# Optimization experiments

Measured on AMD Instinct MI355X. Metric: run time of the kernel, lower is better.

## Reference

```python
import jax, jax.numpy as jnp
import numpy as np

N_NODES = 327680      # 8192 graphs * 40 nodes/graph
N_EDGES = 2621440     # avg degree 8
NODES_PER_GRAPH = 40


def _lin(k, fan_in, fan_out):
    s = 1.0 / np.sqrt(fan_in)
    return jax.random.uniform(k, (fan_in, fan_out), jnp.float32, -s, s)


def setup_inputs() -> dict:
    key = jax.random.key(0)
    ks = jax.random.split(key, 12)
    x = jax.random.normal(ks[0], (N_NODES, 58), jnp.float32)
    edge_index = jax.random.randint(ks[1], (2, N_EDGES), 0, N_NODES, dtype=jnp.int32)
    return {
        "x": x,
        "edge_index": edge_index,
        "W1": _lin(ks[2], 58, 96),  "b1": jnp.zeros((96,), jnp.float32),
        "W2": _lin(ks[3], 96, 48),  "b2": jnp.zeros((48,), jnp.float32),
        "l1_w": _lin(ks[4], 40 * 48, 256), "l1_b": jnp.zeros((256,), jnp.float32),
        "l2_w": _lin(ks[5], 256, 64),      "l2_b": jnp.zeros((64,), jnp.float32),
        "l3_w": _lin(ks[6], 64, 1),        "l3_b": jnp.zeros((1,), jnp.float32),
    }


def gcn_conv(x, src, dst, W, b, n):
    # PyG GCNConv: h = X W; out[i] = sum_{(j->i)} d_j^-1/2 d_i^-1/2 h[j] + b
    h = x @ W                                   # [N, out]
    deg = jnp.zeros((n,), h.dtype).at[dst].add(1.0)
    dinv = jnp.where(deg > 0, jax.lax.rsqrt(deg), 0.0)
    norm = dinv[src] * dinv[dst]                # [E]
    out = jax.ops.segment_sum(h[src] * norm[:, None], dst, num_segments=n)
    return out + b


def reference(x, edge_index, W1, b1, W2, b2, l1_w, l1_b, l2_w, l2_b, l3_w, l3_b):
    n = x.shape[0]
    loop = jnp.arange(n, dtype=edge_index.dtype)        # self-loops (PyG default)
    src = jnp.concatenate([edge_index[0], loop])
    dst = jnp.concatenate([edge_index[1], loop])
    h = jax.nn.relu(gcn_conv(x, src, dst, W1, b1, n))   # dropout is identity in eval
    h = jax.nn.relu(gcn_conv(h, src, dst, W2, b2, n))
    g = h.reshape(n // NODES_PER_GRAPH, NODES_PER_GRAPH * 48)
    g = jax.nn.relu(g @ l1_w + l1_b)
    g = jax.nn.relu(g @ l2_w + l2_b)
    return jax.nn.sigmoid(g @ l3_w + l3_b)              # [B, 1]
```

## Files before the change

kernel.cpp:

```cpp
#include <hip/hip_runtime.h>

#define N_NODES 327680
#define N_EDGES 2621440
#define NGRAPH  8192
#define NB      640
#define BCAPE   4608

typedef unsigned int uint;
typedef unsigned short u16;
typedef __attribute__((ext_vector_type(8))) short s16x8;
typedef __attribute__((ext_vector_type(4))) float f32x4;

__device__ __forceinline__ float bl(uint u){ return __uint_as_float(u << 16); }
__device__ __forceinline__ float bh(uint u){ return __uint_as_float(u & 0xffff0000u); }
__device__ __forceinline__ u16 f2b(float f){
    uint u = __float_as_uint(f);
    u += 0x7fffu + ((u>>16)&1u);
    return (u16)(u>>16);
}
__device__ __forceinline__ uint pk(float a, float b){
    return (uint)f2b(a) | ((uint)f2b(b) << 16);
}


__device__ void tr_tile(const float* __restrict__ in, u16* __restrict__ out,
                        int K, int N, int Kpad, int kb, int nb){
    __shared__ u16 t[64][72];
    for (int i = threadIdx.x; i < 4096; i += 256){
        int k = i >> 6, n = i & 63;
        int gk = kb + k, gn = nb + n;
        float v = (gk < K && gn < N) ? in[(size_t)gk*N + gn] : 0.f;
        t[n][k] = f2b(v);
    }
    __syncthreads();
    for (int i = threadIdx.x; i < 4096; i += 256){
        int n = i >> 6, k = i & 63;
        int gk = kb + k, gn = nb + n;
        if (gn < N && gk < Kpad) out[(size_t)gn*Kpad + gk] = t[n][k];
    }
}

__global__ __launch_bounds__(256) void k_prep(
    const float* __restrict__ W1, const float* __restrict__ W2,
    const float* __restrict__ l1w, const float* __restrict__ l2w,
    u16* __restrict__ w1t, u16* __restrict__ w2t,
    u16* __restrict__ l1wt, u16* __restrict__ l2wt, int* __restrict__ gcur)
{
    int b = blockIdx.x;
    if (b < 120)      tr_tile(l1w, l1wt, 1920, 256, 1920, (b%30)*64, (b/30)*64);
    else if (b < 124) tr_tile(l2w, l2wt, 256,  64,  256,  (b-120)*64, 0);
    else if (b < 126) tr_tile(W1,  w1t,  58,   96,  64,   0, (b-124)*64);
    else if (b < 128) tr_tile(W2,  w2t,  96,   48,  96,   (b-126)*64, 0);
    else {
        for (int i = threadIdx.x; i < NB; i += 256) gcur[i] = 0;
    }
}


__global__ __launch_bounds__(256) void k_partition(
    const int* __restrict__ src, const int* __restrict__ dst,
    int* __restrict__ gcur, uint* __restrict__ staging)
{
    __shared__ int cnt[NB], base_[NB];
    int tid = threadIdx.x;
    for (int i = tid; i < NB; i += 256) cnt[i] = 0;
    __syncthreads();
    int e0 = blockIdx.x*4096;
    int d[16];
    #pragma unroll
    for (int j = 0; j < 16; ++j){
        d[j] = dst[e0 + j*256 + tid];
        atomicAdd(&cnt[d[j] >> 9], 1);
    }
    __syncthreads();
    for (int i = tid; i < NB; i += 256)
        base_[i] = atomicAdd(&gcur[i], cnt[i]);
    __syncthreads();
    for (int i = tid; i < NB; i += 256) cnt[i] = 0;
    __syncthreads();
    #pragma unroll
    for (int j = 0; j < 16; ++j){
        int e = e0 + j*256 + tid;
        int b = d[j] >> 9;
        int r = atomicAdd(&cnt[b], 1);
        staging[(uint)b*BCAPE + base_[b] + r] = (uint)src[e] | ((uint)(d[j] & 511) << 19);
    }
}


__global__ __launch_bounds__(512) void k_bucket(
    const uint* __restrict__ staging, const int* __restrict__ gcur,
    int* __restrict__ rowst, int* __restrict__ rendg, float* __restrict__ dinvg,
    int* __restrict__ csr, int* __restrict__ perm)
{
    __shared__ uint sedge[BCAPE];
    __shared__ int deg[512];
    __shared__ int sc[512];
    __shared__ int cur[512];
    __shared__ int dh[64], dbase[64];
    const int b = blockIdx.x;
    const int tid = threadIdx.x;
    const int lo = b*BCAPE;
    int cnt = gcur[b];
    if (cnt > BCAPE) cnt = BCAPE;
    deg[tid] = 0;
    if (tid < 64) dh[tid] = 0;
    __syncthreads();
    for (int t = tid; t < cnt; t += 512){
        uint ed = staging[lo + t];
        sedge[t] = ed;
        atomicAdd(&deg[ed >> 19], 1);
    }
    __syncthreads();
    int d = deg[tid];
    sc[tid] = d;
    __syncthreads();
    for (int o = 1; o < 512; o <<= 1){
        int v = (tid >= o) ? sc[tid-o] : 0;
        __syncthreads();
        sc[tid] += v;
        __syncthreads();
    }
    int incl = sc[tid];
    int excl = incl - d;
    int gnode = b*512 + tid;
    rowst[gnode] = lo + excl;
    rendg[gnode] = lo + incl;
    dinvg[gnode] = 1.0f / sqrtf((float)(d + 1));
    cur[tid] = lo + excl;
    int bin = min(d, 63);
    atomicAdd(&dh[bin], 1);
    __syncthreads();
    if (tid == 0){
        int a = 0;
        #pragma unroll
        for (int i = 0; i < 64; ++i){ dbase[i] = a; a += dh[i]; dh[i] = 0; }
    }
    __syncthreads();
    int pos = dbase[bin] + atomicAdd(&dh[bin], 1);
    perm[b*512 + pos] = gnode;
    for (int t = tid; t < cnt; t += 512){
        uint ed = sedge[t];
        int p = atomicAdd(&cur[ed >> 19], 1);
        csr[p] = (int)(ed & 0x7FFFFu);
    }
}


__global__ void k_prescale2(const float* __restrict__ x, const float* __restrict__ dinv,
                            uint* __restrict__ xs32){
    int gid = blockIdx.x*256 + threadIdx.x;
    int node = gid >> 5, c = gid & 31;
    float dv = dinv[node];
    float a = 0.f, b = 0.f;
    if (c < 29){
        float2 v = *(const float2*)&x[(size_t)node*58 + 2*c];
        a = v.x * dv; b = v.y * dv;
    }
    xs32[(size_t)node*32 + c] = pk(a, b);
}


template<int BR>
__global__ __launch_bounds__(256) void k_gatherv(
    const int* __restrict__ rs, const int* __restrict__ re,
    const int* __restrict__ csr, const float* __restrict__ dinv,
    const int* __restrict__ perm,
    const uint4* __restrict__ feat4,
    const float* __restrict__ bias,
    u16* __restrict__ out)
{
    int slot = (blockIdx.x*256 + threadIdx.x) >> 3;
    int c4 = threadIdx.x & 7;
    int node = perm[slot];
    uint4 u = feat4[((uint)node << 3) + c4];
    float a0 = bl(u.x), a1 = bh(u.x), a2 = bl(u.y), a3 = bh(u.y);
    float a4 = bl(u.z), a5 = bh(u.z), a6 = bl(u.w), a7 = bh(u.w);
    int e = rs[node];
    const int e1 = re[node];
    while (e < e1){
        const int last = e1 - 1;
        int idx[8];
        #pragma unroll
        for (int k = 0; k < 8; ++k) idx[k] = csr[min(e + k, last)];
        uint4 uu[8];
        #pragma unroll
        for (int k = 0; k < 8; ++k) uu[k] = feat4[((uint)idx[k] << 3) + c4];
        #pragma unroll
        for (int k = 0; k < 8; ++k){
            if (e + k < e1){
                a0 += bl(uu[k].x); a1 += bh(uu[k].x);
                a2 += bl(uu[k].y); a3 += bh(uu[k].y);
                a4 += bl(uu[k].z); a5 += bh(uu[k].z);
                a6 += bl(uu[k].w); a7 += bh(uu[k].w);
            }
        }
        e += 8;
    }
    float di = dinv[node];
    a0 *= di; a1 *= di; a2 *= di; a3 *= di;
    a4 *= di; a5 *= di; a6 *= di; a7 *= di;
    if (BR){
        if (c4 < 6){
            float4 bz0 = *(const float4*)&bias[8*c4];
            float4 bz1 = *(const float4*)&bias[8*c4 + 4];
            a0 = fmaxf(a0 + bz0.x, 0.f); a1 = fmaxf(a1 + bz0.y, 0.f);
            a2 = fmaxf(a2 + bz0.z, 0.f); a3 = fmaxf(a3 + bz0.w, 0.f);
            a4 = fmaxf(a4 + bz1.x, 0.f); a5 = fmaxf(a5 + bz1.y, 0.f);
            a6 = fmaxf(a6 + bz1.z, 0.f); a7 = fmaxf(a7 + bz1.w, 0.f);
            uint4 w;
            w.x = pk(a0,a1); w.y = pk(a2,a3); w.z = pk(a4,a5); w.w = pk(a6,a7);
            *(uint4*)&out[(size_t)node*48 + c4*8] = w;
        }
    } else {
        uint4 w;
        w.x = pk(a0,a1); w.y = pk(a2,a3); w.z = pk(a4,a5); w.w = pk(a6,a7);
        *(uint4*)&out[(size_t)node*64 + c4*8] = w;
    }
}


__global__ __launch_bounds__(256) void k_conv_mlp(
    const u16* __restrict__ A,
    const u16* __restrict__ w1t,
    const float* __restrict__ b1,
    const u16* __restrict__ w2t,
    const float* __restrict__ dinv,
    u16* __restrict__ ts)
{
    __shared__ __align__(16) u16 As[64][72];
    __shared__ __align__(16) u16 Bt1[96][72];
    __shared__ __align__(16) u16 Bt2[48][104];
    __shared__ __align__(16) u16 sh1[64][104];
    __shared__ float sb1[96];
    const int tid = threadIdx.x;
    {
        const u16* Ab = A + (size_t)blockIdx.x*64*64;
        for (int i = tid; i < 512; i += 256){
            int r = i >> 3, s = i & 7;
            *(uint4*)&As[r][s*8] = *(const uint4*)&Ab[r*64 + s*8];
        }
    }
    for (int i = tid; i < 768; i += 256){
        int n = i >> 3, s = i & 7;
        *(uint4*)&Bt1[n][s*8] = *(const uint4*)&w1t[n*64 + s*8];
    }
    for (int i = tid; i < 576; i += 256){
        int n = i / 12, s = i % 12;
        *(uint4*)&Bt2[n][s*8] = *(const uint4*)&w2t[n*96 + s*8];
    }
    if (tid < 96) sb1[tid] = b1[tid];
    __syncthreads();

    const int wv = tid >> 6, l = tid & 63;
    const int lr = l & 15, lg = l >> 4;
    const int r0 = wv*16;

    f32x4 acc1[6] = {};
    #pragma unroll
    for (int s = 0; s < 2; ++s){
        s16x8 af = *(const s16x8*)&As[r0+lr][s*32 + lg*8];
        #pragma unroll
        for (int t = 0; t < 6; ++t){
            s16x8 bf = *(const s16x8*)&Bt1[t*16+lr][s*32 + lg*8];
            acc1[t] = __builtin_amdgcn_mfma_f32_16x16x32_bf16(af, bf, acc1[t], 0, 0, 0);
        }
    }
    #pragma unroll
    for (int t = 0; t < 6; ++t){
        int col = t*16 + lr;
        float bias = sb1[col];
        #pragma unroll
        for (int r = 0; r < 4; ++r)
            sh1[r0 + lg*4 + r][col] = f2b(fmaxf(acc1[t][r] + bias, 0.f));
    }
    __syncthreads();

    f32x4 acc2[3] = {};
    #pragma unroll
    for (int s = 0; s < 3; ++s){
        s16x8 af = *(const s16x8*)&sh1[r0+lr][s*32 + lg*8];
        #pragma unroll
        for (int t = 0; t < 3; ++t){
            s16x8 bf = *(const s16x8*)&Bt2[t*16+lr][s*32 + lg*8];
            acc2[t] = __builtin_amdgcn_mfma_f32_16x16x32_bf16(af, bf, acc2[t], 0, 0, 0);
        }
    }
    size_t gbase = (size_t)blockIdx.x*64;
    #pragma unroll
    for (int r = 0; r < 4; ++r){
        size_t row = gbase + r0 + lg*4 + r;
        float dv = dinv[row];
        #pragma unroll
        for (int t = 0; t < 3; ++t)
            ts[row*64 + t*16 + lr] = f2b(acc2[t][r] * dv);
        ts[row*64 + 48 + lr] = 0;
    }
}


__global__ __launch_bounds__(256) void k_head(
    const u16* __restrict__ A,
    const u16* __restrict__ l1wt,
    const float* __restrict__ l1b,
    const u16* __restrict__ l2wt,
    const float* __restrict__ l2b,
    const float* __restrict__ l3w, const float* __restrict__ l3b,
    float* __restrict__ out)
{
    __shared__ __align__(16) u16 As[32][72];
    __shared__ __align__(16) u16 Bt[256][72];
    __shared__ float part[32][2];
    u16 (*sh1)[264] = (u16(*)[264])&Bt[0][0];
    const int tid = threadIdx.x;
    const int g0 = blockIdx.x*32;
    const int w = tid >> 6, l = tid & 63;
    const int lr = l & 15, lg = l >> 4;
    const int r0 = (w & 1)*16;
    const int c0 = (w >> 1)*128;
    f32x4 acc[8] = {};
    for (int k0 = 0; k0 < 1920; k0 += 64){
        __syncthreads();
        {
            int r = tid >> 3, s = tid & 7;
            *(uint4*)&As[r][s*8] = *(const uint4*)&A[(size_t)(g0+r)*1920 + k0 + s*8];
        }
        for (int i = tid; i < 2048; i += 256){
            int n = i >> 3, s = i & 7;
            *(uint4*)&Bt[n][s*8] = *(const uint4*)&l1wt[(size_t)n*1920 + k0 + s*8];
        }
        __syncthreads();
        #pragma unroll
        for (int s = 0; s < 2; ++s){
            s16x8 af = *(const s16x8*)&As[r0+lr][s*32 + lg*8];
            #pragma unroll
            for (int t = 0; t < 8; ++t){
                s16x8 bf = *(const s16x8*)&Bt[c0 + t*16 + lr][s*32 + lg*8];
                acc[t] = __builtin_amdgcn_mfma_f32_16x16x32_bf16(af, bf, acc[t], 0, 0, 0);
            }
        }
    }
    __syncthreads();
    #pragma unroll
    for (int t = 0; t < 8; ++t){
        int col = c0 + t*16 + lr;
        float bs = l1b[col];
        #pragma unroll
        for (int r = 0; r < 4; ++r)
            sh1[r0 + lg*4 + r][col] = f2b(fmaxf(acc[t][r] + bs, 0.f));
    }
    __syncthreads();
    f32x4 acc2[2] = {};
    #pragma unroll
    for (int s = 0; s < 8; ++s){
        s16x8 af = *(const s16x8*)&sh1[r0+lr][s*32 + lg*8];
        #pragma unroll
        for (int t = 0; t < 2; ++t){
            int col = (w>>1)*32 + t*16 + lr;
            s16x8 bf = *(const s16x8*)&l2wt[(size_t)col*256 + s*32 + lg*8];
            acc2[t] = __builtin_amdgcn_mfma_f32_16x16x32_bf16(af, bf, acc2[t], 0, 0, 0);
        }
    }
    float p[4];
    #pragma unroll
    for (int r = 0; r < 4; ++r){
        p[r] = 0.f;
        #pragma unroll
        for (int t = 0; t < 2; ++t){
            int col = (w>>1)*32 + t*16 + lr;
            p[r] += fmaxf(acc2[t][r] + l2b[col], 0.f) * l3w[col];
        }
    }
    #pragma unroll
    for (int o = 1; o < 16; o <<= 1){
        #pragma unroll
        for (int r = 0; r < 4; ++r) p[r] += __shfl_xor(p[r], o);
    }
    if (lr == 0){
        #pragma unroll
        for (int r = 0; r < 4; ++r)
            part[r0 + lg*4 + r][w>>1] = p[r];
    }
    __syncthreads();
    if (tid < 32)
        out[g0 + tid] = 1.0f / (1.0f + expf(-(part[tid][0] + part[tid][1] + l3b[0])));
}

extern "C" void kernel_launch(void* const* d_in, const int* in_sizes, int n_in,
                              void* d_out, int out_size, void* d_ws, size_t ws_size,
                              hipStream_t stream){
    const float* x   = (const float*)d_in[0];
    const int*   ei  = (const int*)  d_in[1];
    const int*   src = ei;
    const int*   dst = ei + N_EDGES;
    const float* W1  = (const float*)d_in[2];
    const float* b1  = (const float*)d_in[3];
    const float* W2  = (const float*)d_in[4];
    const float* b2  = (const float*)d_in[5];
    const float* l1w = (const float*)d_in[6];
    const float* l1b = (const float*)d_in[7];
    const float* l2w = (const float*)d_in[8];
    const float* l2b = (const float*)d_in[9];
    const float* l3w = (const float*)d_in[10];
    const float* l3b = (const float*)d_in[11];
    float* out = (float*)d_out;

    char* w = (char*)d_ws;
    auto alloc = [&](size_t bytes){ void* p = (void*)w; w += (bytes + 255) & ~(size_t)255; return p; };
    float* dinv   = (float*)alloc((size_t)N_NODES*4);
    int*   rowst  = (int*)  alloc((size_t)N_NODES*4);
    int*   rend   = (int*)  alloc((size_t)N_NODES*4);
    int*   perm   = (int*)  alloc((size_t)N_NODES*4);
    int*   gcur   = (int*)  alloc(NB*4);
    u16*   w1t    = (u16*)  alloc(96*64*2);
    u16*   w2t    = (u16*)  alloc(48*96*2);
    u16*   l1wt   = (u16*)  alloc((size_t)256*1920*2);
    u16*   l2wt   = (u16*)  alloc((size_t)64*256*2);
    int*   csr    = (int*)  alloc((size_t)NB*BCAPE*4);
    char*  BUF_A  = (char*) alloc((size_t)N_NODES*64*2);
    char*  BUF_B  = (char*) alloc((size_t)N_NODES*64*2);
    char*  BUF_C  = (char*) alloc((size_t)N_NODES*64*2);

    u16*   agg1    = (u16*)BUF_A;
    u16*   agg2    = (u16*)BUF_A;
    uint*  staging = (uint*)BUF_B;
    uint*  xs32    = (uint*)BUF_B;
    u16*   ts      = (u16*)BUF_C;

    k_prep     <<<129, 256, 0, stream>>>(W1, W2, l1w, l2w, w1t, w2t, l1wt, l2wt, gcur);

    k_partition<<<640, 256, 0, stream>>>(src, dst, gcur, staging);
    k_bucket   <<<640, 512, 0, stream>>>(staging, gcur, rowst, rend, dinv, csr, perm);

    k_prescale2  <<<40960, 256, 0, stream>>>(x, dinv, xs32);
    k_gatherv<0> <<<10240, 256, 0, stream>>>(rowst, rend, csr, dinv, perm,
                                             (const uint4*)xs32, nullptr, agg1);
    k_conv_mlp   <<<5120,  256, 0, stream>>>(agg1, w1t, b1, w2t, dinv, ts);

    k_gatherv<1> <<<10240, 256, 0, stream>>>(rowst, rend, csr, dinv, perm,
                                             (const uint4*)ts, b2, agg2);

    k_head       <<<256,   256, 0, stream>>>(agg2, l1wt, l1b, l2wt, l2b, l3w, l3b, out);
}
```

Measured before the change: 341.3 us.

## Fuse prescale into bucket, gather1 into conv MLP, and shrink layer-2 feature stride

Folds the x prescale into k_bucket using shared-memory dinv, and fuses the first neighbor gather with the two small MFMA GEMMs so the aggregated tile goes straight to LDS instead of through global memory. k_fused1 scatters its output through perm into a compact 48-wide ts layout. The second gather then reads 12-byte uint3 rows instead of padded 16-byte rows, which cuts gather traffic. Costs: k_fused1 blocks now carry irregular gather latency alongside a large LDS footprint, which may lower occupancy. Buffer aliasing is also replaced with separate allocations.

```diff
diff --git a/kernel.cpp b/kernel.cpp
--- a/kernel.cpp
+++ b/kernel.cpp
@@ -90,14 +90,16 @@
 
 __global__ __launch_bounds__(512) void k_bucket(
     const uint* __restrict__ staging, const int* __restrict__ gcur,
+    const float* __restrict__ x,
     int* __restrict__ rowst, int* __restrict__ rendg, float* __restrict__ dinvg,
-    int* __restrict__ csr, int* __restrict__ perm)
+    int* __restrict__ csr, int* __restrict__ perm, uint* __restrict__ xs32)
 {
     __shared__ uint sedge[BCAPE];
     __shared__ int deg[512];
     __shared__ int sc[512];
     __shared__ int cur[512];
     __shared__ int dh[64], dbase[64];
+    __shared__ float sdinv[512];
     const int b = blockIdx.x;
     const int tid = threadIdx.x;
     const int lo = b*BCAPE;
@@ -124,9 +126,11 @@
     int incl = sc[tid];
     int excl = incl - d;
     int gnode = b*512 + tid;
+    float dv = 1.0f / sqrtf((float)(d + 1));
     rowst[gnode] = lo + excl;
     rendg[gnode] = lo + incl;
-    dinvg[gnode] = 1.0f / sqrtf((float)(d + 1));
+    dinvg[gnode] = dv;
+    sdinv[tid] = dv;
     cur[tid] = lo + excl;
     int bin = min(d, 63);
     atomicAdd(&dh[bin], 1);
@@ -144,38 +148,150 @@
         int p = atomicAdd(&cur[ed >> 19], 1);
         csr[p] = (int)(ed & 0x7FFFFu);
     }
-}
-
-
-__global__ void k_prescale2(const float* __restrict__ x, const float* __restrict__ dinv,
-                            uint* __restrict__ xs32){
-    int gid = blockIdx.x*256 + threadIdx.x;
-    int node = gid >> 5, c = gid & 31;
-    float dv = dinv[node];
-    float a = 0.f, b = 0.f;
-    if (c < 29){
-        float2 v = *(const float2*)&x[(size_t)node*58 + 2*c];
-        a = v.x * dv; b = v.y * dv;
-    }
-    xs32[(size_t)node*32 + c] = pk(a, b);
-}
-
-
-template<int BR>
-__global__ __launch_bounds__(256) void k_gatherv(
+    const size_t n0 = (size_t)b*512;
+    for (int i = tid; i < 512*32; i += 512){
+        int n = i >> 5, c = i & 31;
+        float dvn = sdinv[n];
+        float a = 0.f, bb = 0.f;
+        if (c < 29){
+            float2 v = *(const float2*)&x[(n0 + n)*58 + 2*c];
+            a = v.x * dvn; bb = v.y * dvn;
+        }
+        xs32[(n0 + n)*32 + c] = pk(a, bb);
+    }
+}
+
+
+__global__ __launch_bounds__(256) void k_fused1(
     const int* __restrict__ rs, const int* __restrict__ re,
     const int* __restrict__ csr, const float* __restrict__ dinv,
     const int* __restrict__ perm,
     const uint4* __restrict__ feat4,
+    const u16* __restrict__ w1t,
+    const float* __restrict__ b1,
+    const u16* __restrict__ w2t,
+    u16* __restrict__ ts)
+{
+    __shared__ __align__(16) u16 As[64][72];
+    __shared__ __align__(16) u16 Bt1[96][72];
+    __shared__ __align__(16) u16 Bt2[48][104];
+    __shared__ __align__(16) u16 sh1[64][104];
+    __shared__ float sb1[96];
+    __shared__ int   snode[64];
+    __shared__ float sdv[64];
+    const int tid = threadIdx.x;
+
+    for (int i = tid; i < 768; i += 256){
+        int n = i >> 3, s = i & 7;
+        *(uint4*)&Bt1[n][s*8] = *(const uint4*)&w1t[n*64 + s*8];
+    }
+    for (int i = tid; i < 576; i += 256){
+        int n = i / 12, s = i % 12;
+        *(uint4*)&Bt2[n][s*8] = *(const uint4*)&w2t[n*96 + s*8];
+    }
+    if (tid < 96) sb1[tid] = b1[tid];
+
+    {
+        const int g = tid >> 3, c4 = tid & 7;
+        #pragma unroll
+        for (int pass = 0; pass < 2; ++pass){
+            int row = pass*32 + g;
+            int node = perm[blockIdx.x*64 + row];
+            float di = dinv[node];
+            uint4 u = feat4[((uint)node << 3) + c4];
+            float a0 = bl(u.x), a1 = bh(u.x), a2 = bl(u.y), a3 = bh(u.y);
+            float a4 = bl(u.z), a5 = bh(u.z), a6 = bl(u.w), a7 = bh(u.w);
+            int e = rs[node];
+            const int e1 = re[node];
+            while (e < e1){
+                const int last = e1 - 1;
+                int idx[8];
+                #pragma unroll
+                for (int k = 0; k < 8; ++k) idx[k] = csr[min(e + k, last)];
+                uint4 uu[8];
+                #pragma unroll
+                for (int k = 0; k < 8; ++k) uu[k] = feat4[((uint)idx[k] << 3) + c4];
+                #pragma unroll
+                for (int k = 0; k < 8; ++k){
+                    if (e + k < e1){
+                        a0 += bl(uu[k].x); a1 += bh(uu[k].x);
+                        a2 += bl(uu[k].y); a3 += bh(uu[k].y);
+                        a4 += bl(uu[k].z); a5 += bh(uu[k].z);
+                        a6 += bl(uu[k].w); a7 += bh(uu[k].w);
+                    }
+                }
+                e += 8;
+            }
+            a0 *= di; a1 *= di; a2 *= di; a3 *= di;
+            a4 *= di; a5 *= di; a6 *= di; a7 *= di;
+            if (c4 == 0){ snode[row] = node; sdv[row] = di; }
+            uint4 w;
+            w.x = pk(a0,a1); w.y = pk(a2,a3); w.z = pk(a4,a5); w.w = pk(a6,a7);
+            *(uint4*)&As[row][c4*8] = w;
+        }
+    }
+    __syncthreads();
+
+    const int wv = tid >> 6, l = tid & 63;
+    const int lr = l & 15, lg = l >> 4;
+    const int r0 = wv*16;
+
+    f32x4 acc1[6] = {};
+    #pragma unroll
+    for (int s = 0; s < 2; ++s){
+        s16x8 af = *(const s16x8*)&As[r0+lr][s*32 + lg*8];
+        #pragma unroll
+        for (int t = 0; t < 6; ++t){
+            s16x8 bf = *(const s16x8*)&Bt1[t*16+lr][s*32 + lg*8];
+            acc1[t] = __builtin_amdgcn_mfma_f32_16x16x32_bf16(af, bf, acc1[t], 0, 0, 0);
+        }
+    }
+    #pragma unroll
+    for (int t = 0; t < 6; ++t){
+        int col = t*16 + lr;
+        float bias = sb1[col];
+        #pragma unroll
+        for (int r = 0; r < 4; ++r)
+            sh1[r0 + lg*4 + r][col] = f2b(fmaxf(acc1[t][r] + bias, 0.f));
+    }
+    __syncthreads();
+
+    f32x4 acc2[3] = {};
+    #pragma unroll
+    for (int s = 0; s < 3; ++s){
+        s16x8 af = *(const s16x8*)&sh1[r0+lr][s*32 + lg*8];
+        #pragma unroll
+        for (int t = 0; t < 3; ++t){
+            s16x8 bf = *(const s16x8*)&Bt2[t*16+lr][s*32 + lg*8];
+            acc2[t] = __builtin_amdgcn_mfma_f32_16x16x32_bf16(af, bf, acc2[t], 0, 0, 0);
+        }
+    }
+    #pragma unroll
+    for (int r = 0; r < 4; ++r){
+        int row = r0 + lg*4 + r;
+        size_t node = (size_t)snode[row];
+        float dv = sdv[row];
+        #pragma unroll
+        for (int t = 0; t < 3; ++t)
+            ts[node*48 + t*16 + lr] = f2b(acc2[t][r] * dv);
+    }
+}
+
+
+__global__ __launch_bounds__(256) void k_gather2(
+    const int* __restrict__ rs, const int* __restrict__ re,
+    const int* __restrict__ csr, const float* __restrict__ dinv,
+    const int* __restrict__ perm,
+    const uint* __restrict__ feat,
     const float* __restrict__ bias,
-    u16* __restrict__ out)
+    uint* __restrict__ out)
 {
     int slot = (blockIdx.x*256 + threadIdx.x) >> 3;
     int c4 = threadIdx.x & 7;
     int node = perm[slot];
-    uint4 u = feat4[((uint)node << 3) + c4];
+    uint3 u = *(const uint3*)&feat[(size_t)node*24 + c4*3];
     float a0 = bl(u.x), a1 = bh(u.x), a2 = bl(u.y), a3 = bh(u.y);
-    float a4 = bl(u.z), a5 = bh(u.z), a6 = bl(u.w), a7 = bh(u.w);
+    float a4 = bl(u.z), a5 = bh(u.z);
     int e = rs[node];
     const int e1 = re[node];
     while (e < e1){
@@ -183,119 +299,29 @@
         int idx[8];
         #pragma unroll
         for (int k = 0; k < 8; ++k) idx[k] = csr[min(e + k, last)];
-        uint4 uu[8];
-        #pragma unroll
-        for (int k = 0; k < 8; ++k) uu[k] = feat4[((uint)idx[k] << 3) + c4];
+        uint3 uu[8];
+        #pragma unroll
+        for (int k = 0; k < 8; ++k) uu[k] = *(const uint3*)&feat[(size_t)idx[k]*24 + c4*3];
         #pragma unroll
         for (int k = 0; k < 8; ++k){
             if (e + k < e1){
                 a0 += bl(uu[k].x); a1 += bh(uu[k].x);
                 a2 += bl(uu[k].y); a3 += bh(uu[k].y);
                 a4 += bl(uu[k].z); a5 += bh(uu[k].z);
-                a6 += bl(uu[k].w); a7 += bh(uu[k].w);
             }
         }
         e += 8;
     }
     float di = dinv[node];
-    a0 *= di; a1 *= di; a2 *= di; a3 *= di;
-    a4 *= di; a5 *= di; a6 *= di; a7 *= di;
-    if (BR){
-        if (c4 < 6){
-            float4 bz0 = *(const float4*)&bias[8*c4];
-            float4 bz1 = *(const float4*)&bias[8*c4 + 4];
-            a0 = fmaxf(a0 + bz0.x, 0.f); a1 = fmaxf(a1 + bz0.y, 0.f);
-            a2 = fmaxf(a2 + bz0.z, 0.f); a3 = fmaxf(a3 + bz0.w, 0.f);
-            a4 = fmaxf(a4 + bz1.x, 0.f); a5 = fmaxf(a5 + bz1.y, 0.f);
-            a6 = fmaxf(a6 + bz1.z, 0.f); a7 = fmaxf(a7 + bz1.w, 0.f);
-            uint4 w;
-            w.x = pk(a0,a1); w.y = pk(a2,a3); w.z = pk(a4,a5); w.w = pk(a6,a7);
-            *(uint4*)&out[(size_t)node*48 + c4*8] = w;
-        }
-    } else {
-        uint4 w;
-        w.x = pk(a0,a1); w.y = pk(a2,a3); w.z = pk(a4,a5); w.w = pk(a6,a7);
-        *(uint4*)&out[(size_t)node*64 + c4*8] = w;
-    }
-}
-
-
-__global__ __launch_bounds__(256) void k_conv_mlp(
-    const u16* __restrict__ A,
-    const u16* __restrict__ w1t,
-    const float* __restrict__ b1,
-    const u16* __restrict__ w2t,
-    const float* __restrict__ dinv,
-    u16* __restrict__ ts)
-{
-    __shared__ __align__(16) u16 As[64][72];
-    __shared__ __align__(16) u16 Bt1[96][72];
-    __shared__ __align__(16) u16 Bt2[48][104];
-    __shared__ __align__(16) u16 sh1[64][104];
-    __shared__ float sb1[96];
-    const int tid = threadIdx.x;
-    {
-        const u16* Ab = A + (size_t)blockIdx.x*64*64;
-        for (int i = tid; i < 512; i += 256){
-            int r = i >> 3, s = i & 7;
-            *(uint4*)&As[r][s*8] = *(const uint4*)&Ab[r*64 + s*8];
-        }
-    }
-    for (int i = tid; i < 768; i += 256){
-        int n = i >> 3, s = i & 7;
-        *(uint4*)&Bt1[n][s*8] = *(const uint4*)&w1t[n*64 + s*8];
-    }
-    for (int i = tid; i < 576; i += 256){
-        int n = i / 12, s = i % 12;
-        *(uint4*)&Bt2[n][s*8] = *(const uint4*)&w2t[n*96 + s*8];
-    }
-    if (tid < 96) sb1[tid] = b1[tid];
-    __syncthreads();
-
-    const int wv = tid >> 6, l = tid & 63;
-    const int lr = l & 15, lg = l >> 4;
-    const int r0 = wv*16;
-
-    f32x4 acc1[6] = {};
-    #pragma unroll
-    for (int s = 0; s < 2; ++s){
-        s16x8 af = *(const s16x8*)&As[r0+lr][s*32 + lg*8];
-        #pragma unroll
-        for (int t = 0; t < 6; ++t){
-            s16x8 bf = *(const s16x8*)&Bt1[t*16+lr][s*32 + lg*8];
-            acc1[t] = __builtin_amdgcn_mfma_f32_16x16x32_bf16(af, bf, acc1[t], 0, 0, 0);
-        }
-    }
-    #pragma unroll
-    for (int t = 0; t < 6; ++t){
-        int col = t*16 + lr;
-        float bias = sb1[col];
-        #pragma unroll
-        for (int r = 0; r < 4; ++r)
-            sh1[r0 + lg*4 + r][col] = f2b(fmaxf(acc1[t][r] + bias, 0.f));
-    }
-    __syncthreads();
-
-    f32x4 acc2[3] = {};
-    #pragma unroll
-    for (int s = 0; s < 3; ++s){
-        s16x8 af = *(const s16x8*)&sh1[r0+lr][s*32 + lg*8];
-        #pragma unroll
-        for (int t = 0; t < 3; ++t){
-            s16x8 bf = *(const s16x8*)&Bt2[t*16+lr][s*32 + lg*8];
-            acc2[t] = __builtin_amdgcn_mfma_f32_16x16x32_bf16(af, bf, acc2[t], 0, 0, 0);
-        }
-    }
-    size_t gbase = (size_t)blockIdx.x*64;
-    #pragma unroll
-    for (int r = 0; r < 4; ++r){
-        size_t row = gbase + r0 + lg*4 + r;
-        float dv = dinv[row];
-        #pragma unroll
-        for (int t = 0; t < 3; ++t)
-            ts[row*64 + t*16 + lr] = f2b(acc2[t][r] * dv);
-        ts[row*64 + 48 + lr] = 0;
-    }
+    a0 = fmaxf(a0*di + bias[6*c4+0], 0.f);
+    a1 = fmaxf(a1*di + bias[6*c4+1], 0.f);
+    a2 = fmaxf(a2*di + bias[6*c4+2], 0.f);
+    a3 = fmaxf(a3*di + bias[6*c4+3], 0.f);
+    a4 = fmaxf(a4*di + bias[6*c4+4], 0.f);
+    a5 = fmaxf(a5*di + bias[6*c4+5], 0.f);
+    uint3 w;
+    w.x = pk(a0,a1); w.y = pk(a2,a3); w.z = pk(a4,a5);
+    *(uint3*)&out[(size_t)node*24 + c4*3] = w;
 }
 
 
@@ -407,38 +433,31 @@
 
     char* w = (char*)d_ws;
     auto alloc = [&](size_t bytes){ void* p = (void*)w; w += (bytes + 255) & ~(size_t)255; return p; };
-    float* dinv   = (float*)alloc((size_t)N_NODES*4);
-    int*   rowst  = (int*)  alloc((size_t)N_NODES*4);
-    int*   rend   = (int*)  alloc((size_t)N_NODES*4);
-    int*   perm   = (int*)  alloc((size_t)N_NODES*4);
-    int*   gcur   = (int*)  alloc(NB*4);
-    u16*   w1t    = (u16*)  alloc(96*64*2);
-    u16*   w2t    = (u16*)  alloc(48*96*2);
-    u16*   l1wt   = (u16*)  alloc((size_t)256*1920*2);
-    u16*   l2wt   = (u16*)  alloc((size_t)64*256*2);
-    int*   csr    = (int*)  alloc((size_t)NB*BCAPE*4);
-    char*  BUF_A  = (char*) alloc((size_t)N_NODES*64*2);
-    char*  BUF_B  = (char*) alloc((size_t)N_NODES*64*2);
-    char*  BUF_C  = (char*) alloc((size_t)N_NODES*64*2);
-
-    u16*   agg1    = (u16*)BUF_A;
-    u16*   agg2    = (u16*)BUF_A;
-    uint*  staging = (uint*)BUF_B;
-    uint*  xs32    = (uint*)BUF_B;
-    u16*   ts      = (u16*)BUF_C;
+    float* dinv    = (float*)alloc((size_t)N_NODES*4);
+    int*   rowst   = (int*)  alloc((size_t)N_NODES*4);
+    int*   rend    = (int*)  alloc((size_t)N_NODES*4);
+    int*   perm    = (int*)  alloc((size_t)N_NODES*4);
+    int*   gcur    = (int*)  alloc(NB*4);
+    u16*   w1t     = (u16*)  alloc(96*64*2);
+    u16*   w2t     = (u16*)  alloc(48*96*2);
+    u16*   l1wt    = (u16*)  alloc((size_t)256*1920*2);
+    u16*   l2wt    = (u16*)  alloc((size_t)64*256*2);
+    int*   csr     = (int*)  alloc((size_t)NB*BCAPE*4);
+    uint*  staging = (uint*) alloc((size_t)NB*BCAPE*4);
+    uint*  xs32    = (uint*) alloc((size_t)N_NODES*32*4);
+    u16*   ts      = (u16*)  alloc((size_t)N_NODES*48*2);
+    u16*   agg2    = (u16*)  alloc((size_t)N_NODES*48*2);
 
     k_prep     <<<129, 256, 0, stream>>>(W1, W2, l1w, l2w, w1t, w2t, l1wt, l2wt, gcur);
 
     k_partition<<<640, 256, 0, stream>>>(src, dst, gcur, staging);
-    k_bucket   <<<640, 512, 0, stream>>>(staging, gcur, rowst, rend, dinv, csr, perm);
-
-    k_prescale2  <<<40960, 256, 0, stream>>>(x, dinv, xs32);
-    k_gatherv<0> <<<10240, 256, 0, stream>>>(rowst, rend, csr, dinv, perm,
-                                             (const uint4*)xs32, nullptr, agg1);
-    k_conv_mlp   <<<5120,  256, 0, stream>>>(agg1, w1t, b1, w2t, dinv, ts);
-
-    k_gatherv<1> <<<10240, 256, 0, stream>>>(rowst, rend, csr, dinv, perm,
-                                             (const uint4*)ts, b2, agg2);
-
-    k_head       <<<256,   256, 0, stream>>>(agg2, l1wt, l1b, l2wt, l2b, l3w, l3b, out);
-}
+    k_bucket   <<<640, 512, 0, stream>>>(staging, gcur, x, rowst, rend, dinv, csr, perm, xs32);
+
+    k_fused1   <<<5120, 256, 0, stream>>>(rowst, rend, csr, dinv, perm,
+                                          (const uint4*)xs32, w1t, b1, w2t, ts);
+
+    k_gather2  <<<10240, 256, 0, stream>>>(rowst, rend, csr, dinv, perm,
+                                           (const uint*)ts, b2, (uint*)agg2);
+
+    k_head     <<<256, 256, 0, stream>>>(agg2, l1wt, l1b, l2wt, l2b, l3w, l3b, out);
+}
```

Result: slower. 351.5 us (+3.0%).
